# Kernel optimization log

Hardware: AMD Instinct MI355X
Metric: run time of the kernel (lower is better)

Reference implementation:

```python
import jax, jax.numpy as jnp
import numpy as np

B, N, E = 2, 10000, 160000
NODE_DIM, EDGE_DIM, HIDDEN = 128, 64, 256


def setup_inputs() -> dict:
    key = jax.random.key(0)
    ks = jax.random.split(key, 12)
    def lin(k, fan_in, fan_out):
        return jax.random.normal(k, (fan_in, fan_out), dtype=jnp.float32) / np.sqrt(fan_in)
    msg_in = 2 * NODE_DIM + EDGE_DIM   # 320
    upd_in = NODE_DIM + HIDDEN         # 384
    return {
        "node_features": jax.random.normal(ks[0], (B, N, NODE_DIM), dtype=jnp.float32),
        "edge_indices": jax.random.randint(ks[1], (B, E, 2), 0, N, dtype=jnp.int32),
        "edge_features": jax.random.normal(ks[2], (B, E, EDGE_DIM), dtype=jnp.float32),
        "W1m": lin(ks[3], msg_in, HIDDEN),  "b1m": jnp.zeros((HIDDEN,), jnp.float32),
        "W2m": lin(ks[4], HIDDEN, HIDDEN),  "b2m": jnp.zeros((HIDDEN,), jnp.float32),
        "W1u": lin(ks[5], upd_in, HIDDEN),  "b1u": jnp.zeros((HIDDEN,), jnp.float32),
        "W2u": lin(ks[6], HIDDEN, NODE_DIM), "b2u": jnp.zeros((NODE_DIM,), jnp.float32),
    }


def reference(node_features, edge_indices, edge_features,
              W1m, b1m, W2m, b2m, W1u, b1u, W2u, b2u):
    # node_features: [B, N, D]; edge_indices: [B, E, 2]; edge_features: [B, E, F]
    b, n, d = node_features.shape
    e = edge_indices.shape[1]
    src_idx = edge_indices[..., 0]  # [B, E]
    dst_idx = edge_indices[..., 1]  # [B, E]
    # batched gather of endpoint features
    src = jnp.take_along_axis(node_features, src_idx[..., None], axis=1)  # [B, E, D]
    dst = jnp.take_along_axis(node_features, dst_idx[..., None], axis=1)  # [B, E, D]
    msg_in = jnp.concatenate([src, dst, edge_features], axis=-1)          # [B, E, 2D+F]
    h = jax.nn.gelu(jnp.einsum("bei,ih->beh", msg_in, W1m) + b1m)
    messages = jnp.einsum("beh,ho->beo", h, W2m) + b2m                    # [B, E, H]
    # scatter-add into destination node buckets (flatten batch for segment_sum)
    flat_dst = (dst_idx + (jnp.arange(b, dtype=dst_idx.dtype)[:, None] * n)).reshape(-1)
    aggregated = jax.ops.segment_sum(
        messages.reshape(b * e, -1), flat_dst, num_segments=b * n
    ).reshape(b, n, -1)                                                   # [B, N, H]
    upd_in = jnp.concatenate([node_features, aggregated], axis=-1)        # [B, N, D+H]
    u = jax.nn.gelu(jnp.einsum("bni,ih->bnh", upd_in, W1u) + b1u)
    return jnp.einsum("bnh,ho->bno", u, W2u) + b2u                        # [B, N, D]
```

## Files before the change

kernel.cpp:

```cpp
#include <hip/hip_runtime.h>
#include <hip/hip_bf16.h>
#include <math.h>

#define BATCH   2
#define N_NODES 10000
#define E_EDGES 160000
#define BN      (BATCH * N_NODES)
#define BE      (BATCH * E_EDGES)
#define ND      128
#define ED      64
#define HID     256
#define K1      320
#define K2      256
#define K1U     384
#define NOUT    128
#define TM      64
#define TME     64
#define LDH     264
#define SCAN_BLOCKS ((BN + 1023) / 1024)

typedef __attribute__((ext_vector_type(8))) short bf16x8;
typedef __attribute__((ext_vector_type(4))) float f32x4;

__device__ float          g_P[(size_t)BN * 512];
__device__ unsigned short g_nodef_bf[(size_t)BN * ND];
__device__ unsigned short g_w1ut[K1U * HID];
__device__ unsigned short g_w2ut[K2 * NOUT];

__device__ __forceinline__ float gelu_tanh(float x) {
    float u = 0.7978845608028654f * (x + 0.044715f * x * x * x);
    float e = __expf(2.0f * u);
    float t = 1.0f - 2.0f * __builtin_amdgcn_rcpf(e + 1.0f);
    return 0.5f * x * (1.0f + t);
}

__device__ __forceinline__ unsigned short f2bf(float f) {
    __hip_bfloat16 h = __float2bfloat16(f);
    return *reinterpret_cast<unsigned short*>(&h);
}

__device__ __forceinline__ float bf2f(unsigned short u) {
    unsigned int x = ((unsigned int)u) << 16;
    return *reinterpret_cast<float*>(&x);
}


__global__ __launch_bounds__(256) void f32_to_bf16_vec(
    const float* __restrict__ in, int n4)
{
    int i = blockIdx.x * blockDim.x + threadIdx.x;
    if (i < n4) {
        float4 v = ((const float4*)in)[i];
        ushort4 o;
        o.x = f2bf(v.x); o.y = f2bf(v.y); o.z = f2bf(v.z); o.w = f2bf(v.w);
        ((ushort4*)g_nodef_bf)[i] = o;
    }
}

__global__ __launch_bounds__(256) void prep_weights(
    const float* __restrict__ W1m, unsigned short* __restrict__ w1t,
    const float* __restrict__ W2m, unsigned short* __restrict__ w2t,
    const float* __restrict__ W1u, const float* __restrict__ W2u)
{
    int id = blockIdx.x * blockDim.x + threadIdx.x;
    if (id < K1 * HID) {
        int k = id % K1, n = id / K1;
        w1t[id] = f2bf(W1m[(size_t)k * HID + n]);
    }
    if (id < K2 * HID) {
        int k = id % K2, n = id / K2;
        w2t[id] = f2bf(W2m[(size_t)k * HID + n]);
    }
    if (id < K1U * HID) {
        int k = id % K1U, n = id / K1U;
        g_w1ut[id] = f2bf(W1u[(size_t)k * HID + n]);
    }
    if (id < K2 * NOUT) {
        int k = id % K2, n = id / K2;
        g_w2ut[id] = f2bf(W2u[(size_t)k * NOUT + n]);
    }
}

__global__ __launch_bounds__(256) void dst_hist(
    const int* __restrict__ eidx, int* __restrict__ hist)
{
    int e = blockIdx.x * blockDim.x + threadIdx.x;
    if (e < BE) {
        int dst = eidx[2 * e + 1];
        int b   = e / E_EDGES;
        atomicAdd(&hist[b * N_NODES + dst], 1);
    }
}


__global__ __launch_bounds__(1024) void scan_partial(
    const int* __restrict__ hist, int* __restrict__ offs, int* __restrict__ bsum)
{
    __shared__ int buf[1024];
    int tid = threadIdx.x;
    int i   = blockIdx.x * 1024 + tid;
    int v   = (i < BN) ? hist[i] : 0;
    buf[tid] = v;
    __syncthreads();
    #pragma unroll
    for (int d = 1; d < 1024; d <<= 1) {
        int t = (tid >= d) ? buf[tid - d] : 0;
        __syncthreads();
        buf[tid] += t;
        __syncthreads();
    }
    int incl = buf[tid];
    if (i < BN) offs[i] = incl - v;
    if (tid == 1023) bsum[blockIdx.x] = incl;
}

__global__ __launch_bounds__(1024) void scan_add(
    int* __restrict__ offs, const int* __restrict__ bsum)
{
    __shared__ int sbase;
    int tid = threadIdx.x;
    if (tid < 64) {
        int v = (tid < blockIdx.x && tid < SCAN_BLOCKS) ? bsum[tid] : 0;
        #pragma unroll
        for (int d = 32; d > 0; d >>= 1) v += __shfl_down(v, d);
        if (tid == 0) sbase = v;
    }
    __syncthreads();
    int i = blockIdx.x * 1024 + tid;
    if (i < BN) offs[i] += sbase;
}

__global__ __launch_bounds__(256) void dst_scatter(
    const int* __restrict__ eidx, int* __restrict__ offs, int* __restrict__ perm)
{
    int e = blockIdx.x * blockDim.x + threadIdx.x;
    if (e < BE) {
        int dst  = eidx[2 * e + 1];
        int b    = e / E_EDGES;
        int pos  = atomicAdd(&offs[b * N_NODES + dst], 1);
        perm[pos] = e;
    }
}

__global__ __launch_bounds__(512, 2) void pgemm(const unsigned short* __restrict__ w1t)
{
    const int tid  = threadIdx.x;
    const int wave = tid >> 6;
    const int lane = tid & 63;
    const int quad = lane >> 4;
    const int r16  = lane & 15;
    const int n0   = blockIdx.x * TM;

    const int jb   = (wave & 3) * 64;
    const int koff = (wave < 4) ? 0 : 128;
    const int cb   = (wave < 4) ? 0 : 256;

    f32x4 acc[4][4];
    #pragma unroll
    for (int mt = 0; mt < 4; ++mt)
        #pragma unroll
        for (int nt = 0; nt < 4; ++nt)
            acc[mt][nt] = (f32x4){0.f, 0.f, 0.f, 0.f};

    for (int ks = 0; ks < ND / 32; ++ks) {
        bf16x8 wf[4], nf[4];
        #pragma unroll
        for (int nt = 0; nt < 4; ++nt)
            wf[nt] = *(const bf16x8*)&w1t[(size_t)(jb + nt * 16 + r16) * K1
                                          + koff + ks * 32 + quad * 8];
        #pragma unroll
        for (int mt = 0; mt < 4; ++mt) {
            int row = n0 + mt * 16 + r16; if (row >= BN) row = BN - 1;
            nf[mt] = *(const bf16x8*)&g_nodef_bf[(size_t)row * ND + ks * 32 + quad * 8];
        }
        #pragma unroll
        for (int mt = 0; mt < 4; ++mt)
            #pragma unroll
            for (int nt = 0; nt < 4; ++nt)
                acc[mt][nt] = __builtin_amdgcn_mfma_f32_16x16x32_bf16(
                    wf[nt], nf[mt], acc[mt][nt], 0, 0, 0);
    }

    #pragma unroll
    for (int nt = 0; nt < 4; ++nt) {
        int j0 = cb + jb + nt * 16 + quad * 4;
        #pragma unroll
        for (int mt = 0; mt < 4; ++mt) {
            int m = n0 + mt * 16 + r16;
            if (m < BN) {
                float4 v = {acc[mt][nt][0], acc[mt][nt][1],
                            acc[mt][nt][2], acc[mt][nt][3]};
                *(float4*)&g_P[(size_t)m * 512 + j0] = v;
            }
        }
    }
}

#define EK_SE   0
#define EK_SH   8192
#define EK_SMEM (8192 + TME * LDH * 2)

__global__ __launch_bounds__(512, 6) void edge_mlp_mfma(
    const int*            __restrict__ eidx,
    const float*          __restrict__ edgef,
    const int*            __restrict__ perm,
    const unsigned short* __restrict__ w1t,
    const float*          __restrict__ b1m,
    const unsigned short* __restrict__ w2t,
    const float*          __restrict__ b2m,
    float* __restrict__ agg)
{
    __shared__ __align__(16) char smem[EK_SMEM];
    unsigned short* sE = (unsigned short*)(smem + EK_SE);
    unsigned short* sH = (unsigned short*)(smem + EK_SH);
    __shared__ int s_src[TME];
    __shared__ int s_dst[TME];
    __shared__ int s_eid[TME];

    const int tid  = threadIdx.x;
    const int wave = tid >> 6;
    const int lane = tid & 63;
    const int quad = lane >> 4;
    const int r16  = lane & 15;
    const int be0  = blockIdx.x * TME;

    if (tid < TME) {
        int eid = perm[be0 + tid];
        int b   = eid / E_EDGES;
        int2 se = ((const int2*)eidx)[eid];
        s_eid[tid] = eid;
        s_src[tid] = b * N_NODES + se.x;
        s_dst[tid] = b * N_NODES + se.y;
    }

    const unsigned short* wB1 = w1t + (size_t)(wave * 32) * K1 + 256;
    bf16x8 wf00 = *(const bf16x8*)&wB1[(size_t)r16        * K1 + quad * 8];
    bf16x8 wf01 = *(const bf16x8*)&wB1[(size_t)r16        * K1 + 32 + quad * 8];
    bf16x8 wf10 = *(const bf16x8*)&wB1[(size_t)(16 + r16) * K1 + quad * 8];
    bf16x8 wf11 = *(const bf16x8*)&wB1[(size_t)(16 + r16) * K1 + 32 + quad * 8];

    __syncthreads();

    {
        int row = tid >> 3;
        int c0  = (tid & 7) * 8;
        const float* fp = edgef + (size_t)s_eid[row] * ED + c0;
        float4 v0 = *(const float4*)fp;
        float4 v1 = *(const float4*)(fp + 4);
        ushort4 o0, o1;
        o0.x = f2bf(v0.x); o0.y = f2bf(v0.y); o0.z = f2bf(v0.z); o0.w = f2bf(v0.w);
        o1.x = f2bf(v1.x); o1.y = f2bf(v1.y); o1.z = f2bf(v1.z); o1.w = f2bf(v1.w);
        int p2 = c0 >> 5, kk = c0 & 31;
        *(ushort4*)&sE[p2 * 2048 + row * 32 + kk]     = o0;
        *(ushort4*)&sE[p2 * 2048 + row * 32 + kk + 4] = o1;
    }
    __syncthreads();

    f32x4 acc[4][2];
    #pragma unroll
    for (int mt = 0; mt < 4; ++mt)
        #pragma unroll
        for (int nt = 0; nt < 2; ++nt)
            acc[mt][nt] = (f32x4){0.f, 0.f, 0.f, 0.f};

    #pragma unroll
    for (int mt = 0; mt < 4; ++mt) {
        bf16x8 e0 = *(const bf16x8*)&sE[(mt * 16 + r16) * 32 + quad * 8];
        bf16x8 e1 = *(const bf16x8*)&sE[2048 + (mt * 16 + r16) * 32 + quad * 8];
        acc[mt][0] = __builtin_amdgcn_mfma_f32_16x16x32_bf16(wf00, e0, acc[mt][0], 0, 0, 0);
        acc[mt][1] = __builtin_amdgcn_mfma_f32_16x16x32_bf16(wf10, e0, acc[mt][1], 0, 0, 0);
        acc[mt][0] = __builtin_amdgcn_mfma_f32_16x16x32_bf16(wf01, e1, acc[mt][0], 0, 0, 0);
        acc[mt][1] = __builtin_amdgcn_mfma_f32_16x16x32_bf16(wf11, e1, acc[mt][1], 0, 0, 0);
    }

    {
        float4 bb[2];
        bb[0] = *(const float4*)&b1m[wave * 32 + quad * 4];
        bb[1] = *(const float4*)&b1m[wave * 32 + 16 + quad * 4];
        #pragma unroll
        for (int mt = 0; mt < 4; ++mt) {
            int m = mt * 16 + r16;
            const float* pS = &g_P[(size_t)s_src[m] * 512];
            const float* pD = &g_P[(size_t)s_dst[m] * 512 + 256];
            #pragma unroll
            for (int nt = 0; nt < 2; ++nt) {
                int n0 = wave * 32 + nt * 16 + quad * 4;
                float4 vs = *(const float4*)(pS + n0);
                float4 vd = *(const float4*)(pD + n0);
                ushort4 o;
                o.x = f2bf(gelu_tanh(acc[mt][nt][0] + vs.x + vd.x + bb[nt].x));
                o.y = f2bf(gelu_tanh(acc[mt][nt][1] + vs.y + vd.y + bb[nt].y));
                o.z = f2bf(gelu_tanh(acc[mt][nt][2] + vs.z + vd.z + bb[nt].z));
                o.w = f2bf(gelu_tanh(acc[mt][nt][3] + vs.w + vd.w + bb[nt].w));
                *(ushort4*)&sH[m * LDH + n0] = o;
                acc[mt][nt] = (f32x4){0.f, 0.f, 0.f, 0.f};
            }
        }
    }
    __syncthreads();

    {
        const unsigned short* wB = w2t + (size_t)(wave * 32) * K2;
        bf16x8 bc0 = *(const bf16x8*)&wB[(size_t)r16        * K2 + quad * 8];
        bf16x8 bc1 = *(const bf16x8*)&wB[(size_t)(16 + r16) * K2 + quad * 8];
        #pragma unroll
        for (int ks = 0; ks < K2 / 32; ++ks) {
            bf16x8 bn0 = bc0, bn1 = bc1;
            if (ks + 1 < K2 / 32) {
                bn0 = *(const bf16x8*)&wB[(size_t)r16        * K2 + (ks + 1) * 32 + quad * 8];
                bn1 = *(const bf16x8*)&wB[(size_t)(16 + r16) * K2 + (ks + 1) * 32 + quad * 8];
            }
            bf16x8 hf[4];
            #pragma unroll
            for (int mt = 0; mt < 4; ++mt)
                hf[mt] = *(const bf16x8*)&sH[(mt * 16 + r16) * LDH + ks * 32 + quad * 8];
            #pragma unroll
            for (int mt = 0; mt < 4; ++mt) {
                acc[mt][0] = __builtin_amdgcn_mfma_f32_16x16x32_bf16(
                    bc0, hf[mt], acc[mt][0], 0, 0, 0);
                acc[mt][1] = __builtin_amdgcn_mfma_f32_16x16x32_bf16(
                    bc1, hf[mt], acc[mt][1], 0, 0, 0);
            }
            bc0 = bn0; bc1 = bn1;
        }
    }
    __syncthreads();

    unsigned short* fb = sH;
    {
        float4 bb[2];
        bb[0] = *(const float4*)&b2m[wave * 32 + quad * 4];
        bb[1] = *(const float4*)&b2m[wave * 32 + 16 + quad * 4];
        #pragma unroll
        for (int mt = 0; mt < 4; ++mt) {
            int m = mt * 16 + r16;
            #pragma unroll
            for (int nt = 0; nt < 2; ++nt) {
                int n0 = wave * 32 + nt * 16 + quad * 4;
                ushort4 o;
                o.x = f2bf(acc[mt][nt][0] + bb[nt].x);
                o.y = f2bf(acc[mt][nt][1] + bb[nt].y);
                o.z = f2bf(acc[mt][nt][2] + bb[nt].z);
                o.w = f2bf(acc[mt][nt][3] + bb[nt].w);
                *(ushort4*)&fb[m * LDH + n0] = o;
            }
        }
    }
    __syncthreads();

    {
        const int cc = tid & 255;
        const int r0 = (tid >> 8) * 32;
        int   cur  = s_dst[r0];
        float racc = 0.f;
        for (int mb = 0; mb < 32; mb += 8) {
            float v[8];
            #pragma unroll
            for (int j = 0; j < 8; ++j)
                v[j] = bf2f(fb[(r0 + mb + j) * LDH + cc]);
            #pragma unroll
            for (int j = 0; j < 8; ++j) {
                int d = s_dst[r0 + mb + j];
                if (d != cur) {
                    atomicAdd(&agg[(size_t)cur * HID + cc], racc);
                    cur = d; racc = v[j];
                } else {
                    racc += v[j];
                }
            }
        }
        atomicAdd(&agg[(size_t)cur * HID + cc], racc);
    }
}

__global__ __launch_bounds__(256) void node_mlp_mfma(
    const float* __restrict__ agg,
    const float* __restrict__ b1u,
    const float* __restrict__ b2u,
    float* __restrict__ out)
{
    __shared__ __align__(16) unsigned short sH[TM * LDH];

    const int tid  = threadIdx.x;
    const int wave = tid >> 6;
    const int lane = tid & 63;
    const int quad = lane >> 4;
    const int r16  = lane & 15;
    const int n0   = blockIdx.x * TM;

    f32x4 acc[4][4];
    #pragma unroll
    for (int mt = 0; mt < 4; ++mt)
        #pragma unroll
        for (int nt = 0; nt < 4; ++nt)
            acc[mt][nt] = (f32x4){0.f, 0.f, 0.f, 0.f};

    for (int ks = 0; ks < 4; ++ks) {
        bf16x8 wf[4], nf[4];
        #pragma unroll
        for (int nt = 0; nt < 4; ++nt)
            wf[nt] = *(const bf16x8*)&g_w1ut[(size_t)(wave * 64 + nt * 16 + r16) * K1U
                                             + ks * 32 + quad * 8];
        #pragma unroll
        for (int mt = 0; mt < 4; ++mt) {
            int row = n0 + mt * 16 + r16; if (row >= BN) row = BN - 1;
            nf[mt] = *(const bf16x8*)&g_nodef_bf[(size_t)row * ND + ks * 32 + quad * 8];
        }
        #pragma unroll
        for (int mt = 0; mt < 4; ++mt)
            #pragma unroll
            for (int nt = 0; nt < 4; ++nt)
                acc[mt][nt] = __builtin_amdgcn_mfma_f32_16x16x32_bf16(
                    wf[nt], nf[mt], acc[mt][nt], 0, 0, 0);
    }
    for (int ks = 0; ks < 8; ++ks) {
        bf16x8 wf[4], nf[4];
        #pragma unroll
        for (int nt = 0; nt < 4; ++nt)
            wf[nt] = *(const bf16x8*)&g_w1ut[(size_t)(wave * 64 + nt * 16 + r16) * K1U
                                             + (4 + ks) * 32 + quad * 8];
        #pragma unroll
        for (int mt = 0; mt < 4; ++mt) {
            int row = n0 + mt * 16 + r16; if (row >= BN) row = BN - 1;
            const float* fp = &agg[(size_t)row * HID + ks * 32 + quad * 8];
            float4 v0 = *(const float4*)fp;
            float4 v1 = *(const float4*)(fp + 4);
            union { bf16x8 v; ushort4 u[2]; } cv;
            cv.u[0] = (ushort4){f2bf(v0.x), f2bf(v0.y), f2bf(v0.z), f2bf(v0.w)};
            cv.u[1] = (ushort4){f2bf(v1.x), f2bf(v1.y), f2bf(v1.z), f2bf(v1.w)};
            nf[mt] = cv.v;
        }
        #pragma unroll
        for (int mt = 0; mt < 4; ++mt)
            #pragma unroll
            for (int nt = 0; nt < 4; ++nt)
                acc[mt][nt] = __builtin_amdgcn_mfma_f32_16x16x32_bf16(
                    wf[nt], nf[mt], acc[mt][nt], 0, 0, 0);
    }

    #pragma unroll
    for (int nt = 0; nt < 4; ++nt) {
        int nn0 = wave * 64 + nt * 16 + quad * 4;
        float4 bb = *(const float4*)&b1u[nn0];
        #pragma unroll
        for (int mt = 0; mt < 4; ++mt) {
            int m = mt * 16 + r16;
            ushort4 o;
            o.x = f2bf(gelu_tanh(acc[mt][nt][0] + bb.x));
            o.y = f2bf(gelu_tanh(acc[mt][nt][1] + bb.y));
            o.z = f2bf(gelu_tanh(acc[mt][nt][2] + bb.z));
            o.w = f2bf(gelu_tanh(acc[mt][nt][3] + bb.w));
            *(ushort4*)&sH[m * LDH + nn0] = o;
        }
    }
    __syncthreads();

    f32x4 acc2[4][2];
    #pragma unroll
    for (int mt = 0; mt < 4; ++mt)
        #pragma unroll
        for (int nt = 0; nt < 2; ++nt)
            acc2[mt][nt] = (f32x4){0.f, 0.f, 0.f, 0.f};

    for (int ks = 0; ks < K2 / 32; ++ks) {
        bf16x8 wf2[2], hf[4];
        #pragma unroll
        for (int nt = 0; nt < 2; ++nt)
            wf2[nt] = *(const bf16x8*)&g_w2ut[(size_t)(wave * 32 + nt * 16 + r16) * K2
                                              + ks * 32 + quad * 8];
        #pragma unroll
        for (int mt = 0; mt < 4; ++mt)
            hf[mt] = *(const bf16x8*)&sH[(mt * 16 + r16) * LDH + ks * 32 + quad * 8];
        #pragma unroll
        for (int mt = 0; mt < 4; ++mt)
            #pragma unroll
            for (int nt = 0; nt < 2; ++nt)
                acc2[mt][nt] = __builtin_amdgcn_mfma_f32_16x16x32_bf16(
                    wf2[nt], hf[mt], acc2[mt][nt], 0, 0, 0);
    }

    #pragma unroll
    for (int nt = 0; nt < 2; ++nt) {
        int j0 = wave * 32 + nt * 16 + quad * 4;
        float4 bb = *(const float4*)&b2u[j0];
        #pragma unroll
        for (int mt = 0; mt < 4; ++mt) {
            int row = n0 + mt * 16 + r16;
            if (row < BN) {
                float4 v = {acc2[mt][nt][0] + bb.x, acc2[mt][nt][1] + bb.y,
                            acc2[mt][nt][2] + bb.z, acc2[mt][nt][3] + bb.w};
                *(float4*)&out[(size_t)row * NOUT + j0] = v;
            }
        }
    }
}


extern "C" void kernel_launch(void* const* d_in, const int* in_sizes, int n_in,
                              void* d_out, int out_size, void* d_ws, size_t ws_size,
                              hipStream_t stream) {
    const float* nodef = (const float*)d_in[0];
    const int*   eidx  = (const int*)  d_in[1];
    const float* edgef = (const float*)d_in[2];
    const float* W1m   = (const float*)d_in[3];
    const float* b1m   = (const float*)d_in[4];
    const float* W2m   = (const float*)d_in[5];
    const float* b2m   = (const float*)d_in[6];
    const float* W1u   = (const float*)d_in[7];
    const float* b1u   = (const float*)d_in[8];
    const float* W2u   = (const float*)d_in[9];
    const float* b2u   = (const float*)d_in[10];
    float* out = (float*)d_out;

    char* wsb = (char*)d_ws;
    float* agg = (float*)wsb;
    const size_t AGG_B = (size_t)BN * HID * sizeof(float);

    char* ob = (char*)d_out;
    unsigned short* w1t  = (unsigned short*)(ob + 5120000);
    unsigned short* w2t  = (unsigned short*)(ob + 5283840);
    int* hist            = (int*)(ob + 5414912);
    int* offs            = (int*)(ob + 5494912);
    int* perm            = (int*)(ob + 5574912);
    int* bsum            = (int*)(ob + 6854912);

    hipMemsetAsync(agg, 0, AGG_B, stream);
    hipMemsetAsync(hist, 0, BN * sizeof(int), stream);

    {
        int n4 = BN * ND / 4;
        f32_to_bf16_vec<<<(n4 + 255) / 256, 256, 0, stream>>>(nodef, n4);
    }
    prep_weights<<<(K1U * HID + 255) / 256, 256, 0, stream>>>(
        W1m, w1t, W2m, w2t, W1u, W2u);

    pgemm<<<(BN + TM - 1) / TM, 512, 0, stream>>>(w1t);

    dst_hist<<<(BE + 255) / 256, 256, 0, stream>>>(eidx, hist);
    scan_partial<<<SCAN_BLOCKS, 1024, 0, stream>>>(hist, offs, bsum);
    scan_add<<<SCAN_BLOCKS, 1024, 0, stream>>>(offs, bsum);
    dst_scatter<<<(BE + 255) / 256, 256, 0, stream>>>(eidx, offs, perm);

    edge_mlp_mfma<<<BE / TME, 512, 0, stream>>>(
        eidx, edgef, perm, w1t, b1m, w2t, b2m, agg);

    node_mlp_mfma<<<(BN + TM - 1) / TM, 256, 0, stream>>>(agg, b1u, b2u, out);
}
```

Baseline: 414.0 us.

## Fold edge second-layer linear into node update weights via linearity of segment sum

Since messages are linear in h, the edge kernel now scatter-adds the post-GELU hidden activations directly, and the W2m·W1u product is precomputed into a combined node-update weight with a per-node degree-scaled bias term (hist·b2m·W1u). This removes the second per-edge 256x256 GEMM, which ran over 320k edges, and replaces it with a small weight-product kernel. The histogram is moved to a device global that is zeroed inside the conversion kernel, so one memset goes away. The change shifts bf16 rounding points, because the combined weights are now rounded after multiplication, and node_mlp gains a launch-bounds occupancy hint.

```diff
diff --git a/kernel.cpp b/kernel.cpp
--- a/kernel.cpp
+++ b/kernel.cpp
@@ -24,8 +24,10 @@
 
 __device__ float          g_P[(size_t)BN * 512];
 __device__ unsigned short g_nodef_bf[(size_t)BN * ND];
-__device__ unsigned short g_w1ut[K1U * HID];
+__device__ unsigned short g_w1c[HID * K1U];
 __device__ unsigned short g_w2ut[K2 * NOUT];
+__device__ float          g_bc[HID];
+__device__ int            g_hist[BN];
 
 __device__ __forceinline__ float gelu_tanh(float x) {
     float u = 0.7978845608028654f * (x + 0.044715f * x * x * x);
@@ -55,11 +57,11 @@
         o.x = f2bf(v.x); o.y = f2bf(v.y); o.z = f2bf(v.z); o.w = f2bf(v.w);
         ((ushort4*)g_nodef_bf)[i] = o;
     }
+    if (i < BN) g_hist[i] = 0;
 }
 
 __global__ __launch_bounds__(256) void prep_weights(
     const float* __restrict__ W1m, unsigned short* __restrict__ w1t,
-    const float* __restrict__ W2m, unsigned short* __restrict__ w2t,
     const float* __restrict__ W1u, const float* __restrict__ W2u)
 {
     int id = blockIdx.x * blockDim.x + threadIdx.x;
@@ -67,13 +69,9 @@
         int k = id % K1, n = id / K1;
         w1t[id] = f2bf(W1m[(size_t)k * HID + n]);
     }
-    if (id < K2 * HID) {
-        int k = id % K2, n = id / K2;
-        w2t[id] = f2bf(W2m[(size_t)k * HID + n]);
-    }
-    if (id < K1U * HID) {
-        int k = id % K1U, n = id / K1U;
-        g_w1ut[id] = f2bf(W1u[(size_t)k * HID + n]);
+    if (id < ND * HID) {
+        int k = id % ND, n = id / ND;
+        g_w1c[n * K1U + k] = f2bf(W1u[(size_t)k * HID + n]);
     }
     if (id < K2 * NOUT) {
         int k = id % K2, n = id / K2;
@@ -81,25 +79,43 @@
     }
 }
 
-__global__ __launch_bounds__(256) void dst_hist(
-    const int* __restrict__ eidx, int* __restrict__ hist)
+__global__ __launch_bounds__(256) void prep_wc(
+    const float* __restrict__ W2m, const float* __restrict__ W1u,
+    const float* __restrict__ b2m)
+{
+    int t = blockIdx.x * blockDim.x + threadIdx.x;
+    int n = t & 255;
+    int j = t >> 8;
+    float a = 0.f;
+    for (int o = 0; o < HID; ++o)
+        a += W2m[(size_t)j * HID + o] * W1u[(size_t)(128 + o) * HID + n];
+    g_w1c[n * K1U + 128 + j] = f2bf(a);
+    if (t < HID) {
+        float c = 0.f;
+        for (int o = 0; o < HID; ++o)
+            c += b2m[o] * W1u[(size_t)(128 + o) * HID + t];
+        g_bc[t] = c;
+    }
+}
+
+__global__ __launch_bounds__(256) void dst_hist(const int* __restrict__ eidx)
 {
     int e = blockIdx.x * blockDim.x + threadIdx.x;
     if (e < BE) {
         int dst = eidx[2 * e + 1];
         int b   = e / E_EDGES;
-        atomicAdd(&hist[b * N_NODES + dst], 1);
+        atomicAdd(&g_hist[b * N_NODES + dst], 1);
     }
 }
 
 
 __global__ __launch_bounds__(1024) void scan_partial(
-    const int* __restrict__ hist, int* __restrict__ offs, int* __restrict__ bsum)
+    int* __restrict__ offs, int* __restrict__ bsum)
 {
     __shared__ int buf[1024];
     int tid = threadIdx.x;
     int i   = blockIdx.x * 1024 + tid;
-    int v   = (i < BN) ? hist[i] : 0;
+    int v   = (i < BN) ? g_hist[i] : 0;
     buf[tid] = v;
     __syncthreads();
     #pragma unroll
@@ -206,8 +222,6 @@
     const int*            __restrict__ perm,
     const unsigned short* __restrict__ w1t,
     const float*          __restrict__ b1m,
-    const unsigned short* __restrict__ w2t,
-    const float*          __restrict__ b2m,
     float* __restrict__ agg)
 {
     __shared__ __align__(16) char smem[EK_SMEM];
@@ -293,56 +307,6 @@
                 o.z = f2bf(gelu_tanh(acc[mt][nt][2] + vs.z + vd.z + bb[nt].z));
                 o.w = f2bf(gelu_tanh(acc[mt][nt][3] + vs.w + vd.w + bb[nt].w));
                 *(ushort4*)&sH[m * LDH + n0] = o;
-                acc[mt][nt] = (f32x4){0.f, 0.f, 0.f, 0.f};
-            }
-        }
-    }
-    __syncthreads();
-
-    {
-        const unsigned short* wB = w2t + (size_t)(wave * 32) * K2;
-        bf16x8 bc0 = *(const bf16x8*)&wB[(size_t)r16        * K2 + quad * 8];
-        bf16x8 bc1 = *(const bf16x8*)&wB[(size_t)(16 + r16) * K2 + quad * 8];
-        #pragma unroll
-        for (int ks = 0; ks < K2 / 32; ++ks) {
-            bf16x8 bn0 = bc0, bn1 = bc1;
-            if (ks + 1 < K2 / 32) {
-                bn0 = *(const bf16x8*)&wB[(size_t)r16        * K2 + (ks + 1) * 32 + quad * 8];
-                bn1 = *(const bf16x8*)&wB[(size_t)(16 + r16) * K2 + (ks + 1) * 32 + quad * 8];
-            }
-            bf16x8 hf[4];
-            #pragma unroll
-            for (int mt = 0; mt < 4; ++mt)
-                hf[mt] = *(const bf16x8*)&sH[(mt * 16 + r16) * LDH + ks * 32 + quad * 8];
-            #pragma unroll
-            for (int mt = 0; mt < 4; ++mt) {
-                acc[mt][0] = __builtin_amdgcn_mfma_f32_16x16x32_bf16(
-                    bc0, hf[mt], acc[mt][0], 0, 0, 0);
-                acc[mt][1] = __builtin_amdgcn_mfma_f32_16x16x32_bf16(
-                    bc1, hf[mt], acc[mt][1], 0, 0, 0);
-            }
-            bc0 = bn0; bc1 = bn1;
-        }
-    }
-    __syncthreads();
-
-    unsigned short* fb = sH;
-    {
-        float4 bb[2];
-        bb[0] = *(const float4*)&b2m[wave * 32 + quad * 4];
-        bb[1] = *(const float4*)&b2m[wave * 32 + 16 + quad * 4];
-        #pragma unroll
-        for (int mt = 0; mt < 4; ++mt) {
-            int m = mt * 16 + r16;
-            #pragma unroll
-            for (int nt = 0; nt < 2; ++nt) {
-                int n0 = wave * 32 + nt * 16 + quad * 4;
-                ushort4 o;
-                o.x = f2bf(acc[mt][nt][0] + bb[nt].x);
-                o.y = f2bf(acc[mt][nt][1] + bb[nt].y);
-                o.z = f2bf(acc[mt][nt][2] + bb[nt].z);
-                o.w = f2bf(acc[mt][nt][3] + bb[nt].w);
-                *(ushort4*)&fb[m * LDH + n0] = o;
             }
         }
     }
@@ -357,7 +321,7 @@
             float v[8];
             #pragma unroll
             for (int j = 0; j < 8; ++j)
-                v[j] = bf2f(fb[(r0 + mb + j) * LDH + cc]);
+                v[j] = bf2f(sH[(r0 + mb + j) * LDH + cc]);
             #pragma unroll
             for (int j = 0; j < 8; ++j) {
                 int d = s_dst[r0 + mb + j];
@@ -373,7 +337,7 @@
     }
 }
 
-__global__ __launch_bounds__(256) void node_mlp_mfma(
+__global__ __launch_bounds__(256, 4) void node_mlp_mfma(
     const float* __restrict__ agg,
     const float* __restrict__ b1u,
     const float* __restrict__ b2u,
@@ -399,8 +363,8 @@
         bf16x8 wf[4], nf[4];
         #pragma unroll
         for (int nt = 0; nt < 4; ++nt)
-            wf[nt] = *(const bf16x8*)&g_w1ut[(size_t)(wave * 64 + nt * 16 + r16) * K1U
-                                             + ks * 32 + quad * 8];
+            wf[nt] = *(const bf16x8*)&g_w1c[(size_t)(wave * 64 + nt * 16 + r16) * K1U
+                                            + ks * 32 + quad * 8];
         #pragma unroll
         for (int mt = 0; mt < 4; ++mt) {
             int row = n0 + mt * 16 + r16; if (row >= BN) row = BN - 1;
@@ -417,8 +381,8 @@
         bf16x8 wf[4], nf[4];
         #pragma unroll
         for (int nt = 0; nt < 4; ++nt)
-            wf[nt] = *(const bf16x8*)&g_w1ut[(size_t)(wave * 64 + nt * 16 + r16) * K1U
-                                             + (4 + ks) * 32 + quad * 8];
+            wf[nt] = *(const bf16x8*)&g_w1c[(size_t)(wave * 64 + nt * 16 + r16) * K1U
+                                            + (4 + ks) * 32 + quad * 8];
         #pragma unroll
         for (int mt = 0; mt < 4; ++mt) {
             int row = n0 + mt * 16 + r16; if (row >= BN) row = BN - 1;
@@ -442,14 +406,17 @@
     for (int nt = 0; nt < 4; ++nt) {
         int nn0 = wave * 64 + nt * 16 + quad * 4;
         float4 bb = *(const float4*)&b1u[nn0];
-        #pragma unroll
-        for (int mt = 0; mt < 4; ++mt) {
+        float4 bc = *(const float4*)&g_bc[nn0];
+        #pragma unroll
+        for (int mt = 0; mt < 4; ++mt) {
+            int row = n0 + mt * 16 + r16; if (row >= BN) row = BN - 1;
+            float hv = (float)g_hist[row];
             int m = mt * 16 + r16;
             ushort4 o;
-            o.x = f2bf(gelu_tanh(acc[mt][nt][0] + bb.x));
-            o.y = f2bf(gelu_tanh(acc[mt][nt][1] + bb.y));
-            o.z = f2bf(gelu_tanh(acc[mt][nt][2] + bb.z));
-            o.w = f2bf(gelu_tanh(acc[mt][nt][3] + bb.w));
+            o.x = f2bf(gelu_tanh(acc[mt][nt][0] + bb.x + hv * bc.x));
+            o.y = f2bf(gelu_tanh(acc[mt][nt][1] + bb.y + hv * bc.y));
+            o.z = f2bf(gelu_tanh(acc[mt][nt][2] + bb.z + hv * bc.z));
+            o.w = f2bf(gelu_tanh(acc[mt][nt][3] + bb.w + hv * bc.w));
             *(ushort4*)&sH[m * LDH + nn0] = o;
         }
     }
@@ -518,31 +485,28 @@
 
     char* ob = (char*)d_out;
     unsigned short* w1t  = (unsigned short*)(ob + 5120000);
-    unsigned short* w2t  = (unsigned short*)(ob + 5283840);
-    int* hist            = (int*)(ob + 5414912);
     int* offs            = (int*)(ob + 5494912);
     int* perm            = (int*)(ob + 5574912);
     int* bsum            = (int*)(ob + 6854912);
 
     hipMemsetAsync(agg, 0, AGG_B, stream);
-    hipMemsetAsync(hist, 0, BN * sizeof(int), stream);
 
     {
         int n4 = BN * ND / 4;
         f32_to_bf16_vec<<<(n4 + 255) / 256, 256, 0, stream>>>(nodef, n4);
     }
-    prep_weights<<<(K1U * HID + 255) / 256, 256, 0, stream>>>(
-        W1m, w1t, W2m, w2t, W1u, W2u);
+    prep_weights<<<(K1 * HID + 255) / 256, 256, 0, stream>>>(W1m, w1t, W1u, W2u);
+    prep_wc<<<(HID * HID) / 256, 256, 0, stream>>>(W2m, W1u, b2m);
 
     pgemm<<<(BN + TM - 1) / TM, 512, 0, stream>>>(w1t);
 
-    dst_hist<<<(BE + 255) / 256, 256, 0, stream>>>(eidx, hist);
-    scan_partial<<<SCAN_BLOCKS, 1024, 0, stream>>>(hist, offs, bsum);
+    dst_hist<<<(BE + 255) / 256, 256, 0, stream>>>(eidx);
+    scan_partial<<<SCAN_BLOCKS, 1024, 0, stream>>>(offs, bsum);
     scan_add<<<SCAN_BLOCKS, 1024, 0, stream>>>(offs, bsum);
     dst_scatter<<<(BE + 255) / 256, 256, 0, stream>>>(eidx, offs, perm);
 
     edge_mlp_mfma<<<BE / TME, 512, 0, stream>>>(
-        eidx, edgef, perm, w1t, b1m, w2t, b2m, agg);
+        eidx, edgef, perm, w1t, b1m, agg);
 
     node_mlp_mfma<<<(BN + TM - 1) / TM, 256, 0, stream>>>(agg, b1u, b2u, out);
 }
```

Result: faster. 365.5 us (-11.7%).
